# Optimization experiments

Measured on AMD Instinct MI355X. Metric: run time of the kernel, lower is better.

Reference implementation:

```python
import jax, jax.numpy as jnp
import numpy as np

N_NODES = 50000


def setup_inputs() -> dict:
    key = jax.random.key(0)
    k1, k2, k3, k4, k5, k6 = jax.random.split(key, 6)
    N, E, DIN, DOUT = N_NODES, 800000, 256, 256
    h = jax.random.normal(k1, (N, DIN), dtype=jnp.float32)
    e_w = jax.random.uniform(k2, (E, 1), dtype=jnp.float32)
    src = jax.random.randint(k3, (E,), 0, N, dtype=jnp.int32)
    dst = jax.random.randint(k4, (E,), 0, N, dtype=jnp.int32)
    stdv = 1.0 / np.sqrt(DOUT)
    weight = jax.random.uniform(k5, (DIN, DOUT), dtype=jnp.float32, minval=-stdv, maxval=stdv)
    bias = jax.random.uniform(k6, (DOUT,), dtype=jnp.float32, minval=-stdv, maxval=stdv)
    return {"h": h, "e_w": e_w, "src": src, "dst": dst, "weight": weight, "bias": bias}


def reference(h, e_w, src, dst, weight, bias):
    # u_mul_e: message m_e = h[src_e] * x_e  (edge weight broadcast over feature dim)
    m = h[src] * e_w                      # [E, DIN]
    # sum('m','h'): scatter-add messages to destination nodes
    agg = jax.ops.segment_sum(m, dst, num_segments=h.shape[0])  # [N, DIN]
    # dense GEMM + bias
    return agg @ weight + bias            # [N, DOUT]
```

## Files before the change

### kernel.cpp

```cpp
#include <hip/hip_runtime.h>
#include <hip/hip_bf16.h>


#define DIN 256
#define DOUT 256
#define CAP 64

typedef short bf16x8 __attribute__((ext_vector_type(8)));
typedef float f32x4  __attribute__((ext_vector_type(4)));
typedef unsigned short ushort8v __attribute__((ext_vector_type(8)));
typedef unsigned short ushort4v __attribute__((ext_vector_type(4)));

__device__ __forceinline__ unsigned short f2bf(float f) {
    unsigned u = __float_as_uint(f);
    u = (u + 0x7FFF + ((u >> 16) & 1)) >> 16;
    return (unsigned short)u;
}
__device__ __forceinline__ float bf2f(unsigned short s) {
    return __uint_as_float(((unsigned)s) << 16);
}

__global__ __launch_bounds__(256) void prep_kernel(const float* __restrict__ W,
                                                   unsigned short* __restrict__ WTfrag,
                                                   int* __restrict__ cursors, int N) {
    int gid = blockIdx.x * 256 + threadIdx.x;
    if (gid < 16 * 8 * 64) {
        int lane = gid & 63;
        int tc = gid >> 6;
        int c = tc & 7;
        int t = tc >> 3;
        int q = lane >> 4, l16 = lane & 15;
        int col = t * 16 + l16;
        int krow = c * 32 + q * 8;
        ushort8v v;
#pragma unroll
        for (int j = 0; j < 8; ++j) v[j] = f2bf(W[(size_t)(krow + j) * DOUT + col]);
        *(ushort8v*)(WTfrag + (size_t)gid * 8) = v;
    }
    for (int i = gid; i < N; i += gridDim.x * 256) cursors[i] = 0;
}

__global__ __launch_bounds__(256) void fill_kernel(const int* __restrict__ src,
                                                   const int* __restrict__ dst,
                                                   const float* __restrict__ e_w,
                                                   int* __restrict__ cursors,
                                                   int2* __restrict__ slots, int E) {
    int e = blockIdx.x * blockDim.x + threadIdx.x;
    if (e < E) {
        int d = dst[e];
        int pos = atomicAdd(&cursors[d], 1);
        if (pos < CAP)
            slots[(size_t)d * CAP + pos] = make_int2(src[e], __float_as_int(e_w[e]));
    }
}

__global__ __launch_bounds__(256, 2) void gemm_mfma_kernel(const float* __restrict__ h,
                                                           const unsigned short* __restrict__ WTfrag,
                                                           unsigned short* __restrict__ hW,
                                                           int M, int ntiles) {
    __shared__ unsigned short Af[4 * 8 * 64 * 8];

    int tid  = threadIdx.x;
    int wave = tid >> 6;
    int lane = tid & 63;
    int quad = lane >> 4;
    int l16  = lane & 15;

    bf16x8 breg[4][8];
#pragma unroll
    for (int tq = 0; tq < 4; ++tq)
#pragma unroll
        for (int c = 0; c < 8; ++c)
            breg[tq][c] = *(const bf16x8*)(WTfrag +
                ((size_t)((wave * 4 + tq) * 8 + c) * 64 + lane) * 8);

    for (int tile = blockIdx.x; tile < ntiles; tile += gridDim.x) {
        int row0 = tile * 64;
        __syncthreads();
#pragma unroll
        for (int j = 0; j < 16; ++j) {
            int flat = j * 256 + tid;
            int row  = flat >> 6;
            int col4 = (flat & 63) << 2;
            int r = row0 + row;
            float4 f = make_float4(0.f, 0.f, 0.f, 0.f);
            if (r < M) f = *(const float4*)(h + (size_t)r * DIN + col4);
            int w = row >> 4, l16r = row & 15;
            int c = col4 >> 5, q = (col4 >> 3) & 3, jj = col4 & 7;
            ushort4v u;
            u[0] = f2bf(f.x); u[1] = f2bf(f.y); u[2] = f2bf(f.z); u[3] = f2bf(f.w);
            *(ushort4v*)&Af[(size_t)(((w * 8 + c) * 64 + q * 16 + l16r) << 3) + jj] = u;
        }
        __syncthreads();

#pragma unroll
        for (int s = 0; s < 4; ++s) {
            f32x4 acc[4];
#pragma unroll
            for (int tq = 0; tq < 4; ++tq) acc[tq] = (f32x4){0.f, 0.f, 0.f, 0.f};
#pragma unroll
            for (int c = 0; c < 8; ++c) {
                bf16x8 a = *(const bf16x8*)&Af[(size_t)((s * 8 + c) * 64 + lane) * 8];
#pragma unroll
                for (int tq = 0; tq < 4; ++tq)
                    acc[tq] = __builtin_amdgcn_mfma_f32_16x16x32_bf16(a, breg[tq][c], acc[tq], 0, 0, 0);
            }
            int r0 = row0 + s * 16;
#pragma unroll
            for (int tq = 0; tq < 4; ++tq) {
#pragma unroll
                for (int r = 0; r < 4; ++r) {
                    int row = r0 + quad * 4 + r;
                    if (row < M)
                        hW[(size_t)row * DOUT + (wave * 4 + tq) * 16 + l16] = f2bf(acc[tq][r]);
                }
            }
        }
    }
}

__global__ __launch_bounds__(256) void gather_kernel(const unsigned short* __restrict__ hW,
                                                     const int2* __restrict__ slots,
                                                     const int* __restrict__ cursors,
                                                     const float* __restrict__ bias,
                                                     float* __restrict__ out, int N) {
    int node = blockIdx.x * 4 + (threadIdx.x >> 6);
    if (node >= N) return;
    int lane = threadIdx.x & 63;
    int len  = cursors[node];
    if (len > CAP) len = CAP;
    const int2* sl = slots + (size_t)node * CAP;

    float a0 = 0.f, a1 = 0.f, a2 = 0.f, a3 = 0.f;
    int i = 0;
    for (; i + 4 <= len; i += 4) {
        int2 m0 = sl[i], m1 = sl[i + 1], m2 = sl[i + 2], m3 = sl[i + 3];
        float w0 = __int_as_float(m0.y), w1 = __int_as_float(m1.y);
        float w2 = __int_as_float(m2.y), w3 = __int_as_float(m3.y);
        ushort4v v0 = *(const ushort4v*)(hW + (size_t)m0.x * DOUT + lane * 4);
        ushort4v v1 = *(const ushort4v*)(hW + (size_t)m1.x * DOUT + lane * 4);
        ushort4v v2 = *(const ushort4v*)(hW + (size_t)m2.x * DOUT + lane * 4);
        ushort4v v3 = *(const ushort4v*)(hW + (size_t)m3.x * DOUT + lane * 4);
        a0 += w0 * bf2f(v0[0]) + w1 * bf2f(v1[0]) + w2 * bf2f(v2[0]) + w3 * bf2f(v3[0]);
        a1 += w0 * bf2f(v0[1]) + w1 * bf2f(v1[1]) + w2 * bf2f(v2[1]) + w3 * bf2f(v3[1]);
        a2 += w0 * bf2f(v0[2]) + w1 * bf2f(v1[2]) + w2 * bf2f(v2[2]) + w3 * bf2f(v3[2]);
        a3 += w0 * bf2f(v0[3]) + w1 * bf2f(v1[3]) + w2 * bf2f(v2[3]) + w3 * bf2f(v3[3]);
    }
    for (; i < len; ++i) {
        int2 m = sl[i];
        float w = __int_as_float(m.y);
        ushort4v v = *(const ushort4v*)(hW + (size_t)m.x * DOUT + lane * 4);
        a0 += w * bf2f(v[0]);
        a1 += w * bf2f(v[1]);
        a2 += w * bf2f(v[2]);
        a3 += w * bf2f(v[3]);
    }
    float4 b = *(const float4*)(bias + lane * 4);
    *(float4*)(out + (size_t)node * DOUT + lane * 4) =
        make_float4(a0 + b.x, a1 + b.y, a2 + b.z, a3 + b.w);
}

extern "C" void kernel_launch(void* const* d_in, const int* in_sizes, int n_in,
                              void* d_out, int out_size, void* d_ws, size_t ws_size,
                              hipStream_t stream) {
    const float* h    = (const float*)d_in[0];
    const float* e_w  = (const float*)d_in[1];
    const int*   src  = (const int*)d_in[2];
    const int*   dst  = (const int*)d_in[3];
    const float* W    = (const float*)d_in[4];
    const float* bias = (const float*)d_in[5];
    float* out = (float*)d_out;

    int N = in_sizes[0] / DIN;
    int E = in_sizes[1];
    int ntiles = (N + 63) / 64;

    char* base = (char*)d_ws;
    unsigned short* WTfrag = (unsigned short*)base;
    size_t off = (size_t)DIN * DOUT * sizeof(unsigned short);
    unsigned short* hW = (unsigned short*)(base + off);
    off += (size_t)N * DOUT * sizeof(unsigned short);
    int* cursors = (int*)(base + off);
    off += (size_t)N * sizeof(int);
    off = (off + 15) & ~(size_t)15;
    int2* slots = (int2*)(base + off);
    off += (size_t)N * CAP * sizeof(int2);

    prep_kernel<<<64, 256, 0, stream>>>(W, WTfrag, cursors, N);
    fill_kernel<<<(E + 255) / 256, 256, 0, stream>>>(src, dst, e_w, cursors, slots, E);
    gemm_mfma_kernel<<<512, 256, 0, stream>>>(h, WTfrag, hW, N, ntiles);
    gather_kernel<<<(N + 3) / 4, 256, 0, stream>>>(hW, slots, cursors, bias, out, N);
}
```

Baseline: 233.0 us.

## Shard gather over column slices with edge-parallel lanes and shuffle reduction

The gather kernel now splits each node's 256 output columns into 8 shards of 32, each handled by its own block. Within a wave, 8 lane groups each process different edges for a 32-column slice, and a cross-lane xor-shuffle reduction combines the partial sums. This raises parallelism and memory-level parallelism for nodes with few edges, at the cost of 8x more blocks, repeated reads of slot and cursor data, and a shuffle reduction. Slot loads and output stores use nontemporal hints.

```diff
diff --git a/kernel.cpp b/kernel.cpp
--- a/kernel.cpp
+++ b/kernel.cpp
@@ -124,40 +124,53 @@
                                                      const int* __restrict__ cursors,
                                                      const float* __restrict__ bias,
                                                      float* __restrict__ out, int N) {
-    int node = blockIdx.x * 4 + (threadIdx.x >> 6);
+    int shard = blockIdx.x & 7;
+    int node  = (blockIdx.x >> 3) * 4 + (threadIdx.x >> 6);
     if (node >= N) return;
     int lane = threadIdx.x & 63;
-    int len  = cursors[node];
+    int g  = lane >> 3;
+    int d8 = lane & 7;
+
+    int len = cursors[node];
     if (len > CAP) len = CAP;
-    const int2* sl = slots + (size_t)node * CAP;
+
+    const long long* slq = (const long long*)(slots + (size_t)node * CAP);
+    const unsigned short* basep = hW + shard * 32 + d8 * 4;
 
     float a0 = 0.f, a1 = 0.f, a2 = 0.f, a3 = 0.f;
-    int i = 0;
-    for (; i + 4 <= len; i += 4) {
-        int2 m0 = sl[i], m1 = sl[i + 1], m2 = sl[i + 2], m3 = sl[i + 3];
-        float w0 = __int_as_float(m0.y), w1 = __int_as_float(m1.y);
-        float w2 = __int_as_float(m2.y), w3 = __int_as_float(m3.y);
-        ushort4v v0 = *(const ushort4v*)(hW + (size_t)m0.x * DOUT + lane * 4);
-        ushort4v v1 = *(const ushort4v*)(hW + (size_t)m1.x * DOUT + lane * 4);
-        ushort4v v2 = *(const ushort4v*)(hW + (size_t)m2.x * DOUT + lane * 4);
-        ushort4v v3 = *(const ushort4v*)(hW + (size_t)m3.x * DOUT + lane * 4);
-        a0 += w0 * bf2f(v0[0]) + w1 * bf2f(v1[0]) + w2 * bf2f(v2[0]) + w3 * bf2f(v3[0]);
-        a1 += w0 * bf2f(v0[1]) + w1 * bf2f(v1[1]) + w2 * bf2f(v2[1]) + w3 * bf2f(v3[1]);
-        a2 += w0 * bf2f(v0[2]) + w1 * bf2f(v1[2]) + w2 * bf2f(v2[2]) + w3 * bf2f(v3[2]);
-        a3 += w0 * bf2f(v0[3]) + w1 * bf2f(v1[3]) + w2 * bf2f(v2[3]) + w3 * bf2f(v3[3]);
-    }
-    for (; i < len; ++i) {
-        int2 m = sl[i];
-        float w = __int_as_float(m.y);
-        ushort4v v = *(const ushort4v*)(hW + (size_t)m.x * DOUT + lane * 4);
-        a0 += w * bf2f(v[0]);
-        a1 += w * bf2f(v[1]);
-        a2 += w * bf2f(v[2]);
-        a3 += w * bf2f(v[3]);
-    }
-    float4 b = *(const float4*)(bias + lane * 4);
-    *(float4*)(out + (size_t)node * DOUT + lane * 4) =
-        make_float4(a0 + b.x, a1 + b.y, a2 + b.z, a3 + b.w);
+    for (int i0 = 0; i0 < len; i0 += 16) {
+        int iA = i0 + g;
+        int iB = iA + 8;
+        bool vA = iA < len;
+        bool vB = iB < len;
+        long long qA = __builtin_nontemporal_load(slq + (vA ? iA : i0));
+        long long qB = __builtin_nontemporal_load(slq + (vB ? iB : i0));
+        int sA = (int)(unsigned)(qA & 0xffffffffll);
+        int sB = (int)(unsigned)(qB & 0xffffffffll);
+        ushort4v rA = *(const ushort4v*)(basep + (size_t)sA * DOUT);
+        ushort4v rB = *(const ushort4v*)(basep + (size_t)sB * DOUT);
+        float wA = vA ? __uint_as_float((unsigned)(qA >> 32)) : 0.f;
+        float wB = vB ? __uint_as_float((unsigned)(qB >> 32)) : 0.f;
+        a0 += wA * bf2f(rA[0]) + wB * bf2f(rB[0]);
+        a1 += wA * bf2f(rA[1]) + wB * bf2f(rB[1]);
+        a2 += wA * bf2f(rA[2]) + wB * bf2f(rB[2]);
+        a3 += wA * bf2f(rA[3]) + wB * bf2f(rB[3]);
+    }
+
+#pragma unroll
+    for (int m = 8; m <= 32; m <<= 1) {
+        a0 += __shfl_xor(a0, m, 64);
+        a1 += __shfl_xor(a1, m, 64);
+        a2 += __shfl_xor(a2, m, 64);
+        a3 += __shfl_xor(a3, m, 64);
+    }
+
+    if (lane < 8) {
+        float4 b = *(const float4*)(bias + shard * 32 + lane * 4);
+        f32x4 v;
+        v[0] = a0 + b.x; v[1] = a1 + b.y; v[2] = a2 + b.z; v[3] = a3 + b.w;
+        __builtin_nontemporal_store(v, (f32x4*)(out + (size_t)node * DOUT + shard * 32 + lane * 4));
+    }
 }
 
 extern "C" void kernel_launch(void* const* d_in, const int* in_sizes, int n_in,
@@ -189,5 +202,5 @@
     prep_kernel<<<64, 256, 0, stream>>>(W, WTfrag, cursors, N);
     fill_kernel<<<(E + 255) / 256, 256, 0, stream>>>(src, dst, e_w, cursors, slots, E);
     gemm_mfma_kernel<<<512, 256, 0, stream>>>(h, WTfrag, hW, N, ntiles);
-    gather_kernel<<<(N + 3) / 4, 256, 0, stream>>>(hW, slots, cursors, bias, out, N);
-}
+    gather_kernel<<<8 * ((N + 3) / 4), 256, 0, stream>>>(hW, slots, cursors, bias, out, N);
+}
```

After: 335.7 us. +44.1%, slower.
